# Kernel optimization log

Hardware: AMD Instinct MI355X
Metric: run time of the kernel (lower is better)

The kernel has to match this reference:

```python
import jax, jax.numpy as jnp
import numpy as np

# B batch, N seq (n_vec), V vocab, D model dim, H heads, DH head dim,
# L depth, WS window size, R landmark rank, C classes
B, N, V, D, H, DH, L, WS, R, C = 4, 4096, 512, 512, 8, 64, 4, 128, 256, 10
FF = 4 * D
SCALE = DH ** -0.5


def _ln(t, g, b, eps=1e-5):
    mu = jnp.mean(t, axis=-1, keepdims=True)
    var = jnp.var(t, axis=-1, keepdims=True)
    return (t - mu) * jax.lax.rsqrt(var + eps) * g + b


def setup_inputs():
    key = jax.random.key(0)
    ks = iter(jax.random.split(key, 16))

    def w(shape, s=0.02):
        return (jax.random.normal(next(ks), shape) * s).astype(jnp.float32)

    return dict(
        x=jax.random.randint(next(ks), (B, N), 0, V, dtype=jnp.int32),
        tok_emb=w((V, D)), pos_emb=w((N, D)),
        ln1_g=jnp.ones((L, D), jnp.float32), ln1_b=jnp.zeros((L, D), jnp.float32),
        Wq=w((L, D, H * DH)), Wkv=w((L, D, 2 * H * DH)), Wp=w((L, DH, R)),
        lln_g=jnp.ones((L, DH), jnp.float32), lln_b=jnp.zeros((L, DH), jnp.float32),
        gln_g=jnp.ones((L, DH), jnp.float32), gln_b=jnp.zeros((L, DH), jnp.float32),
        Wo=w((L, H * DH, D)), bo=jnp.zeros((L, D), jnp.float32),
        ln2_g=jnp.ones((L, D), jnp.float32), ln2_b=jnp.zeros((L, D), jnp.float32),
        W1=w((L, D, FF)), b1=jnp.zeros((L, FF), jnp.float32),
        W2=w((L, FF, D)), b2=jnp.zeros((L, D), jnp.float32),
        lnf_g=jnp.ones((D,), jnp.float32), lnf_b=jnp.zeros((D,), jnp.float32),
        Wlog=w((D, V)), blog=jnp.zeros((V,), jnp.float32),
        Wfin=w((N * V, C), 0.005), bfin=jnp.zeros((C,), jnp.float32),
    )


def _forward(x, tok_emb, pos_emb, ln1_g, ln1_b, Wq, Wkv, Wp, lln_g, lln_b,
             gln_g, gln_b, Wo, bo, ln2_g, ln2_b, W1, b1, W2, b2,
             lnf_g, lnf_b, Wlog, blog, Wfin, bfin):
    h = tok_emb[x] + pos_emb[None, :, :]  # [B,N,D]
    nw = N // WS
    for l in range(L):
        # ---- PreNorm Long-Short attention ----
        y = _ln(h, ln1_g[l], ln1_b[l])
        q = (y @ Wq[l]).reshape(B, N, H, DH).transpose(0, 2, 1, 3) * SCALE  # [B,H,N,DH]
        kv = (y @ Wkv[l]).reshape(B, N, 2, H, DH).transpose(2, 0, 3, 1, 4)
        k, v = kv[0], kv[1]  # [B,H,N,DH]
        # dynamic low-rank landmark projection: softmax over the sequence dim
        p = jax.nn.softmax(jnp.einsum('bhnd,dr->bhnr', k, Wp[l]), axis=2)
        gk = _ln(jnp.einsum('bhnr,bhnd->bhrd', p, k), gln_g[l], gln_b[l])  # [B,H,R,DH]
        gv = _ln(jnp.einsum('bhnr,bhnd->bhrd', p, v), gln_g[l], gln_b[l])
        # DualLN on the short-range (local window) keys/values
        lk = _ln(k, lln_g[l], lln_b[l]).reshape(B, H, nw, WS, DH)
        lv = _ln(v, lln_g[l], lln_b[l]).reshape(B, H, nw, WS, DH)
        lq = q.reshape(B, H, nw, WS, DH)
        sim_l = jnp.einsum('bhnwd,bhnxd->bhnwx', lq, lk)  # [B,H,nw,WS,WS]
        sim_g = jnp.einsum('bhnwd,bhrd->bhnwr', lq, gk)   # [B,H,nw,WS,R]
        attn = jax.nn.softmax(jnp.concatenate([sim_l, sim_g], axis=-1), axis=-1)
        a_l, a_g = attn[..., :WS], attn[..., WS:]
        o = (jnp.einsum('bhnwx,bhnxd->bhnwd', a_l, lv)
             + jnp.einsum('bhnwr,bhrd->bhnwd', a_g, gv))
        o = o.reshape(B, H, N, DH).transpose(0, 2, 1, 3).reshape(B, N, H * DH)
        h = h + o @ Wo[l] + bo[l]
        # ---- PreNorm FeedForward ----
        y = _ln(h, ln2_g[l], ln2_b[l])
        h = h + jax.nn.gelu(y @ W1[l] + b1[l]) @ W2[l] + b2[l]
    logits = _ln(h, lnf_g, lnf_b) @ Wlog + blog  # [B,N,V]
    # FLATTEN pooling head (dropout is identity in eval mode)
    return logits.reshape(B, N * V) @ Wfin + bfin  # [B,C]


def reference(x, tok_emb, pos_emb, ln1_g, ln1_b, Wq, Wkv, Wp, lln_g, lln_b,
              gln_g, gln_b, Wo, bo, ln2_g, ln2_b, W1, b1, W2, b2,
              lnf_g, lnf_b, Wlog, blog, Wfin, bfin):
    return _forward(x, tok_emb, pos_emb, ln1_g, ln1_b, Wq, Wkv, Wp, lln_g, lln_b,
                    gln_g, gln_b, Wo, bo, ln2_g, ln2_b, W1, b1, W2, b2,
                    lnf_g, lnf_b, Wlog, blog, Wfin, bfin)
```

## Files before the change

kernel.cpp:

```cpp
#include <hip/hip_runtime.h>
#include <hip/hip_bf16.h>

typedef unsigned short u16;
typedef __attribute__((ext_vector_type(8))) short short8;
typedef __attribute__((ext_vector_type(4))) float floatx4;

#define FLAG_GELU   1
#define FLAG_ACC    2
#define FLAG_NN     4
#define FLAG_CF32   8
#define FLAG_ATOMIC 16

__device__ __forceinline__ float bf2f(u16 u){
  union { unsigned u; float f; } c; c.u = ((unsigned)u)<<16; return c.f;
}
__device__ __forceinline__ u16 f2bf(float f){
  union { float f; unsigned u; } c; c.f = f;
  unsigned r = (c.u + 0x7fffu + ((c.u>>16)&1u))>>16;
  return (u16)r;
}
__device__ __forceinline__ float rdin(const void* base, long long idx, int flagv){
  return flagv ? ((const float*)base)[idx] : bf2f(((const u16*)base)[idx]);
}
__device__ __forceinline__ float fast_gelu(float x){
  float u = 0.7978845608028654f*(x + 0.044715f*x*x*x);
  float e = __expf(2.f*u);
  float t = 1.f - 2.f/(e+1.f);
  return 0.5f*x*(1.f+t);
}

__global__ void detect_kernel(const void* tok, int* flag){
  __shared__ int cnt;
  if(threadIdx.x==0) cnt=0;
  __syncthreads();
  float v = fabsf(bf2f(((const u16*)tok)[threadIdx.x]));
  int bad = (v < 1e3f) ? 0 : 1;
  atomicAdd(&cnt, bad);
  __syncthreads();
  if(threadIdx.x==0) *flag = (cnt>0) ? 1 : 0;
}

__global__ void cvtT_kernel(const void* src, long long off0, long long zstride, u16* __restrict__ dst,
    long long dzstride, int K, int N, const int* flag){
  __shared__ float tl[32][33];
  int fl = *flag;
  int k0 = blockIdx.x*32, n0 = blockIdx.y*32;
  long long base = off0 + (long long)blockIdx.z*zstride;
  for(int i=threadIdx.y;i<32;i+=8){
    long long idx = base + (long long)(k0+i)*N + n0 + threadIdx.x;
    tl[i][threadIdx.x] = fl ? ((const float*)src)[idx] : bf2f(((const u16*)src)[idx]);
  }
  __syncthreads();
  u16* dz = dst + (long long)blockIdx.z*dzstride;
  for(int i=threadIdx.y;i<32;i+=8)
    dz[(long long)(n0+i)*K + k0 + threadIdx.x] = f2bf(tl[threadIdx.x][i]);
}

__global__ void transposeB_kernel(const u16* __restrict__ in, u16* __restrict__ out,
    long long izs0, long long izs1, int zd, long long ozstride, int ldin, int ldout){
  __shared__ u16 tl[32][33];
  int z = blockIdx.z; int z0 = z/zd, z1 = z - z0*zd;
  const u16* ip = in + z0*izs0 + z1*izs1;
  u16* op = out + (long long)z*ozstride;
  int r0 = blockIdx.x*32, c0 = blockIdx.y*32;
  for(int i=threadIdx.y;i<32;i+=8)
    tl[i][threadIdx.x] = ip[(long long)(r0+i)*ldin + c0 + threadIdx.x];
  __syncthreads();
  for(int i=threadIdx.y;i<32;i+=8)
    op[(long long)(c0+i)*ldout + r0 + threadIdx.x] = tl[threadIdx.x][i];
}

__global__ __launch_bounds__(256) void zerof_kernel(float* p, int n){
  int i = blockIdx.x*256 + threadIdx.x;
  if(i<n) p[i]=0.f;
}

struct GemmP {
  const u16* A; const u16* B; float* Cf; u16* Ch;
  const void* bias; int biasOff; const int* dflag;
  int K, lda, ldb, ldc;
  long long sA0,sA1,sA2,sB0,sB1,sB2,sC0,sC1,sC2;
  int d0,d1; float alpha; int flags; int ksplit;
};

__global__ __launch_bounds__(256) void gemm_kernel(GemmP p){
  __shared__ __align__(16) u16 As[64][40];
  __shared__ __align__(16) u16 Bs[64][40];
  int z = blockIdx.z;
  int i0 = z / p.d0; int rem = z - i0*p.d0; int i1 = rem / p.d1; int i2 = rem - i1*p.d1;
  const u16* A  = p.A + i0*p.sA0 + i1*p.sA1 + i2*p.sA2;
  const u16* Bp = p.B + i0*p.sB0 + i1*p.sB1 + i2*p.sB2;
  long long cb = i0*p.sC0 + i1*p.sC1 + i2*p.sC2;
  int kbeg = 0, kend = p.K;
  if(p.ksplit){ kbeg = i2*p.ksplit; kend = kbeg + p.ksplit; }
  int m0 = blockIdx.x*64, n0 = blockIdx.y*64;
  int t = threadIdx.x, lane = t&63, wave = t>>6;
  int wm = (wave>>1)*32, wn = (wave&1)*32;
  int quad = lane>>4, l16 = lane&15;
  floatx4 zero4 = {0.f,0.f,0.f,0.f};
  floatx4 acc00=zero4, acc01=zero4, acc10=zero4, acc11=zero4;
  int sr = t>>2, sc = (t&3)*8;
  int bkr = t>>3, bnc = (t&7)*8;
  bool nn = (p.flags & FLAG_NN);
  for(int k0=kbeg;k0<kend;k0+=32){
    uint4 av = *(const uint4*)(A + (long long)(m0+sr)*p.lda + (k0+sc));
    uint4 bv;
    if(nn) bv = *(const uint4*)(Bp + (long long)(k0+bkr)*p.ldb + (n0+bnc));
    else   bv = *(const uint4*)(Bp + (long long)(n0+sr)*p.ldb + (k0+sc));
    *(uint4*)&As[sr][sc] = av;
    if(nn){
      u16 tmp[8]; *(uint4*)tmp = bv;
      #pragma unroll
      for(int j=0;j<8;j++) Bs[bnc+j][bkr] = tmp[j];
    } else {
      *(uint4*)&Bs[sr][sc] = bv;
    }
    __syncthreads();
    short8 a0 = *(const short8*)&As[wm+l16][quad*8];
    short8 a1 = *(const short8*)&As[wm+16+l16][quad*8];
    short8 b0 = *(const short8*)&Bs[wn+l16][quad*8];
    short8 b1 = *(const short8*)&Bs[wn+16+l16][quad*8];
    acc00 = __builtin_amdgcn_mfma_f32_16x16x32_bf16(a0,b0,acc00,0,0,0);
    acc01 = __builtin_amdgcn_mfma_f32_16x16x32_bf16(a0,b1,acc01,0,0,0);
    acc10 = __builtin_amdgcn_mfma_f32_16x16x32_bf16(a1,b0,acc10,0,0,0);
    acc11 = __builtin_amdgcn_mfma_f32_16x16x32_bf16(a1,b1,acc11,0,0,0);
    __syncthreads();
  }
  int flagv = p.bias ? *p.dflag : 0;
  #pragma unroll
  for(int mi=0;mi<2;mi++){
    #pragma unroll
    for(int ni=0;ni<2;ni++){
      floatx4 a = (mi==0)?((ni==0)?acc00:acc01):((ni==0)?acc10:acc11);
      int cg = n0 + wn + ni*16 + l16;
      float bv_ = p.bias ? rdin(p.bias, (long long)p.biasOff + cg, flagv) : 0.f;
      #pragma unroll
      for(int e=0;e<4;e++){
        int rg = m0 + wm + mi*16 + quad*4 + e;
        float v = a[e]*p.alpha + bv_;
        if(p.flags & FLAG_GELU) v = fast_gelu(v);
        long long ci = cb + (long long)rg*p.ldc + cg;
        if(p.flags & FLAG_ATOMIC){
          atomicAdd(&p.Cf[ci], v);
        } else if(p.flags & FLAG_CF32){
          float o2 = v; if(p.flags&FLAG_ACC) o2 += p.Cf[ci];
          p.Cf[ci] = o2;
        } else {
          float o2 = v; if(p.flags&FLAG_ACC) o2 += bf2f(p.Ch[ci]);
          p.Ch[ci] = f2bf(o2);
        }
      }
    }
  }
}

struct Gemm128P {
  const u16* A; const u16* B; float* Cf; u16* Ch;
  const void* bias; int biasOff; const int* dflag;
  int K, lda, ldb, ldc; float alpha; int flags;
};

template<int BM>
__global__ __launch_bounds__(512) void gemm2ph_kernel(Gemm128P p){
  constexpr int NA   = BM/64;
  constexpr int HH   = BM/2;
  constexpr int MI   = HH/16;
  constexpr int ABUF = BM*64;
  constexpr int LDSZ = (BM==256) ? 69632 : 49152;
  __shared__ __align__(16) u16 lds[LDSZ];
  u16* As = lds;
  u16* Bs = lds + 2*ABUF;
  int m0 = blockIdx.x*BM, n0 = blockIdx.y*256;
  int t = threadIdx.x, lane = t&63, wave = t>>6;
  int quad = lane>>4, l16 = lane&15;
  int wr = wave>>2, wc = wave&3;
  int rowA = t>>3;
  int colk = (((t&7) ^ (rowA&7)))*8;
  const u16* Asrc[NA];
  const u16* Bsrc[4];
  #pragma unroll
  for(int q=0;q<NA;q++) Asrc[q] = p.A + (long long)(m0 + q*64 + rowA)*p.lda + colk;
  #pragma unroll
  for(int q=0;q<4;q++)  Bsrc[q] = p.B + (long long)(n0 + q*64 + rowA)*p.ldb + colk;
  int nk = p.K >> 6;
  floatx4 acc[MI][4] = {};

  auto stage = [&](int buf, int k0){
    #pragma unroll
    for(int q=0;q<NA;q++)
      __builtin_amdgcn_global_load_lds(
        (const __attribute__((address_space(1))) unsigned int*)(Asrc[q] + k0),
        (__attribute__((address_space(3))) unsigned int*)(As + buf*ABUF + q*4096 + wave*512),
        16, 0, 0);
    #pragma unroll
    for(int q=0;q<4;q++)
      __builtin_amdgcn_global_load_lds(
        (const __attribute__((address_space(1))) unsigned int*)(Bsrc[q] + k0),
        (__attribute__((address_space(3))) unsigned int*)(Bs + buf*16384 + q*4096 + wave*512),
        16, 0, 0);
  };

  stage(0, 0);
  __syncthreads();
  int sw = l16&7;
  for(int kt=0; kt<nk; ++kt){
    int cur = kt&1;
    if(kt+1 < nk) stage(cur^1, (kt+1)*64);
    const u16* Ab = As + cur*ABUF;
    const u16* Bb = Bs + cur*16384;
    #pragma unroll
    for(int ks=0; ks<2; ks++){
      short8 a[MI], b[4];
      #pragma unroll
      for(int i=0;i<MI;i++)
        a[i] = *(const short8*)&Ab[(wr*HH + i*16 + l16)*64 + ((((ks<<2)|quad) ^ sw)<<3)];
      #pragma unroll
      for(int j=0;j<4;j++)
        b[j] = *(const short8*)&Bb[(wc*64 + j*16 + l16)*64 + ((((ks<<2)|quad) ^ sw)<<3)];
      #pragma unroll
      for(int i=0;i<MI;i++)
        #pragma unroll
        for(int j=0;j<4;j++)
          acc[i][j] = __builtin_amdgcn_mfma_f32_16x16x32_bf16(a[i], b[j], acc[i][j],0,0,0);
    }
    __syncthreads();
  }

  int flagv = p.bias ? *p.dflag : 0;
  if(!(p.flags & FLAG_CF32)){
    u16* Ct = lds + wave*(HH*68);
    #pragma unroll
    for(int j=0;j<4;j++){
      int cg = n0 + wc*64 + j*16 + l16;
      float bv_ = p.bias ? rdin(p.bias, (long long)p.biasOff + cg, flagv) : 0.f;
      #pragma unroll
      for(int i=0;i<MI;i++){
        #pragma unroll
        for(int e=0;e<4;e++){
          float v = acc[i][j][e]*p.alpha + bv_;
          if(p.flags & FLAG_GELU) v = fast_gelu(v);
          Ct[(i*16 + quad*4 + e)*68 + j*16 + l16] = f2bf(v);
        }
      }
    }
    int rsub = lane>>3, csub = (lane&7)*8;
    #pragma unroll
    for(int rr=0; rr<HH/8; rr++){
      int row = rr*8 + rsub;
      uint4 v = *(const uint4*)&Ct[row*68 + csub];
      *(uint4*)(p.Ch + (long long)(m0 + wr*HH + row)*p.ldc + (n0 + wc*64 + csub)) = v;
    }
  } else {
    #pragma unroll
    for(int j=0;j<4;j++){
      int cg = n0 + wc*64 + j*16 + l16;
      float bv_ = p.bias ? rdin(p.bias, (long long)p.biasOff + cg, flagv) : 0.f;
      #pragma unroll
      for(int i=0;i<MI;i++){
        #pragma unroll
        for(int e=0;e<4;e++){
          int rg = m0 + wr*HH + i*16 + quad*4 + e;
          float v = acc[i][j][e]*p.alpha + bv_;
          if(p.flags & FLAG_GELU) v = fast_gelu(v);
          long long ci = (long long)rg*p.ldc + cg;
          float o2 = v; if(p.flags&FLAG_ACC) o2 += p.Cf[ci];
          p.Cf[ci] = o2;
        }
      }
    }
  }
}

struct AttnP {
  const u16* q;
  const u16* k;
  const u16* gk;
  const u16* vT;
  const u16* gvT;
  u16* o;
};

__global__ __launch_bounds__(256) void attn_kernel(AttnP p){
  __shared__ __align__(16) u16 S[32*392];
  __shared__ float ssum[32];
  const int SST = 392;
  int qb = blockIdx.x;
  int bh = blockIdx.y;
  int b = bh>>3, hh = bh&7;
  int w = qb>>2;
  int t = threadIdx.x, lane = t&63, wave = t>>6;
  int quad = lane>>4, l16 = lane&15;
  int mbase = qb*32;
  short8 aq[2][2];
  #pragma unroll
  for(int mt=0;mt<2;mt++)
    #pragma unroll
    for(int kc=0;kc<2;kc++)
      aq[mt][kc] = *(const short8*)(p.q + ((long long)b*4096 + mbase + mt*16 + l16)*512 + hh*64 + kc*32 + quad*8);
  #pragma unroll
  for(int i=0;i<6;i++){
    int ct = wave*6 + i;
    short8 bf0, bf1;
    if(ct<8){
      const u16* kr = p.k + ((long long)b*4096 + w*128 + ct*16 + l16)*1024 + hh*64;
      bf0 = *(const short8*)(kr + quad*8);
      bf1 = *(const short8*)(kr + 32 + quad*8);
    } else {
      const u16* gr = p.gk + ((long long)bh*256 + (ct-8)*16 + l16)*64;
      bf0 = *(const short8*)(gr + quad*8);
      bf1 = *(const short8*)(gr + 32 + quad*8);
    }
    #pragma unroll
    for(int mt=0;mt<2;mt++){
      floatx4 acc = {0.f,0.f,0.f,0.f};
      acc = __builtin_amdgcn_mfma_f32_16x16x32_bf16(aq[mt][0], bf0, acc,0,0,0);
      acc = __builtin_amdgcn_mfma_f32_16x16x32_bf16(aq[mt][1], bf1, acc,0,0,0);
      #pragma unroll
      for(int e=0;e<4;e++)
        S[(mt*16 + quad*4 + e)*SST + ct*16 + l16] = f2bf(acc[e]);
    }
  }
  __syncthreads();
  {
    int r = t>>3, seg = t&7;
    u16* Srow = S + r*SST + seg*48;
    u16 buf[48];
    #pragma unroll
    for(int it=0; it<6; it++)
      *(uint4*)(buf + it*8) = *(const uint4*)(Srow + it*8);
    float mmax = -3.4e38f;
    #pragma unroll
    for(int j=0;j<48;j++) mmax = fmaxf(mmax, bf2f(buf[j]));
    mmax = fmaxf(mmax, __shfl_xor(mmax, 1));
    mmax = fmaxf(mmax, __shfl_xor(mmax, 2));
    mmax = fmaxf(mmax, __shfl_xor(mmax, 4));
    float s = 0.f;
    #pragma unroll
    for(int j=0;j<48;j++){ float e_ = __expf(bf2f(buf[j]) - mmax); s += e_; buf[j] = f2bf(e_); }
    #pragma unroll
    for(int it=0; it<6; it++)
      *(uint4*)(Srow + it*8) = *(const uint4*)(buf + it*8);
    s += __shfl_xor(s, 1);
    s += __shfl_xor(s, 2);
    s += __shfl_xor(s, 4);
    if(seg==0) ssum[r] = 1.f/s;
  }
  __syncthreads();
  int dt = wave;
  floatx4 oacc[2] = {};
  for(int kc=0; kc<12; kc++){
    short8 ap0 = *(const short8*)(S + (l16)*SST + kc*32 + quad*8);
    short8 ap1 = *(const short8*)(S + (16 + l16)*SST + kc*32 + quad*8);
    short8 bv;
    if(kc<4)
      bv = *(const short8*)(p.vT + (long long)bh*262144 + (dt*16+l16)*4096 + w*128 + kc*32 + quad*8);
    else
      bv = *(const short8*)(p.gvT + (long long)bh*16384 + (dt*16+l16)*256 + (kc-4)*32 + quad*8);
    oacc[0] = __builtin_amdgcn_mfma_f32_16x16x32_bf16(ap0, bv, oacc[0],0,0,0);
    oacc[1] = __builtin_amdgcn_mfma_f32_16x16x32_bf16(ap1, bv, oacc[1],0,0,0);
  }
  #pragma unroll
  for(int mt=0;mt<2;mt++){
    #pragma unroll
    for(int e=0;e<4;e++){
      int row = mt*16 + quad*4 + e;
      float inv = ssum[row];
      p.o[((long long)b*4096 + mbase + row)*512 + hh*64 + dt*16 + l16] = f2bf(oacc[mt][e]*inv);
    }
  }
}

__global__ __launch_bounds__(256) void embed_kernel(const int* __restrict__ x, const void* tok,
    const void* pos, float* __restrict__ h, const int* flag){
  int i = blockIdx.x*256 + threadIdx.x;
  int flagv = *flag;
  int d = i & 511;
  int n = (i>>9) & 4095;
  int bn = i>>9;
  int tid2 = x[bn];
  h[i] = rdin(tok, (long long)tid2*512 + d, flagv) + rdin(pos, (long long)n*512 + d, flagv);
}

__global__ __launch_bounds__(256) void ln512_kernel(const float* __restrict__ h,
    const void* g, const void* b, int goff, u16* __restrict__ y, const int* flag){
  int row = blockIdx.x;
  int flagv = *flag;
  const float* hr = h + (size_t)row*512;
  int t = threadIdx.x;
  float x0 = hr[t], x1 = hr[t+256];
  float s1 = x0+x1, s2 = x0*x0+x1*x1;
  for(int o=32;o>0;o>>=1){ s1 += __shfl_down(s1,o,64); s2 += __shfl_down(s2,o,64); }
  __shared__ float sh1[4], sh2[4];
  int wv=t>>6, ln=t&63;
  if(ln==0){ sh1[wv]=s1; sh2[wv]=s2; }
  __syncthreads();
  float st = sh1[0]+sh1[1]+sh1[2]+sh1[3];
  float qt = sh2[0]+sh2[1]+sh2[2]+sh2[3];
  float mu = st*(1.f/512.f);
  float var = qt*(1.f/512.f) - mu*mu;
  float inv = rsqrtf(var+1e-5f);
  u16* yr = y + (size_t)row*512;
  yr[t]     = f2bf((x0-mu)*inv*rdin(g,goff+t,flagv)     + rdin(b,goff+t,flagv));
  yr[t+256] = f2bf((x1-mu)*inv*rdin(g,goff+t+256,flagv) + rdin(b,goff+t+256,flagv));
}

__global__ __launch_bounds__(256) void ln64_kernel(const u16* __restrict__ in, const float* __restrict__ inF,
    u16* __restrict__ out, const void* g, const void* b, int goff,
    long long s0, long long s1v, long long s2v, int d0, int d1, const int* flag){
  int r = blockIdx.x*4 + (threadIdx.x>>6);
  int ln = threadIdx.x&63;
  int flagv = *flag;
  int i0 = r/d0; int rem = r - i0*d0; int i1 = rem/d1; int i2 = rem - i1*d1;
  long long off = i0*s0 + i1*s1v + i2*s2v;
  float x = inF ? inF[off+ln] : bf2f(in[off + ln]);
  float s = x, sq = x*x;
  for(int o=32;o>0;o>>=1){ s += __shfl_down(s,o,64); sq += __shfl_down(sq,o,64); }
  s = __shfl(s,0,64); sq = __shfl(sq,0,64);
  float mu = s*(1.f/64.f), var = sq*(1.f/64.f)-mu*mu;
  float inv = rsqrtf(var+1e-5f);
  out[off + ln] = f2bf((x-mu)*inv*rdin(g,goff+ln,flagv) + rdin(b,goff+ln,flagv));
}

__global__ __launch_bounds__(256) void softmax4096_kernel(u16* __restrict__ p){
  u16* pr = p + (size_t)blockIdx.x*4096;
  int t = threadIdx.x;
  u16 tmp[16];
  *(uint4*)tmp     = *(const uint4*)(pr + t*16);
  *(uint4*)(tmp+8) = *(const uint4*)(pr + t*16 + 8);
  float xs[16]; float m=-3.4e38f;
  #pragma unroll
  for(int i=0;i<16;i++){ xs[i]=bf2f(tmp[i]); m=fmaxf(m,xs[i]); }
  for(int o=32;o>0;o>>=1) m = fmaxf(m, __shfl_down(m,o,64));
  __shared__ float sm[4]; __shared__ float sv[4];
  int wv=t>>6, ln=t&63;
  if(ln==0) sm[wv]=m;
  __syncthreads();
  m = fmaxf(fmaxf(sm[0],sm[1]),fmaxf(sm[2],sm[3]));
  float s=0;
  #pragma unroll
  for(int i=0;i<16;i++){ xs[i]=__expf(xs[i]-m); s+=xs[i]; }
  for(int o=32;o>0;o>>=1) s += __shfl_down(s,o,64);
  if(ln==0) sv[wv]=s;
  __syncthreads();
  s = sv[0]+sv[1]+sv[2]+sv[3];
  float inv = 1.f/s;
  #pragma unroll
  for(int i=0;i<16;i++) tmp[i]=f2bf(xs[i]*inv);
  *(uint4*)(pr + t*16)     = *(uint4*)tmp;
  *(uint4*)(pr + t*16 + 8) = *(uint4*)(tmp+8);
}

__global__ void zero40_kernel(float* p){ if(threadIdx.x<40) p[threadIdx.x]=0.f; }

__global__ __launch_bounds__(256) void head_kernel(const float* __restrict__ logits,
    const void* wfin, float* __restrict__ part, const int* flag){
  int b = blockIdx.x>>8, chunk = blockIdx.x&255;
  int flagv = *flag;
  const float* lr = logits + (size_t)b*2097152 + (size_t)chunk*8192;
  long long jbase = (long long)chunk*8192;
  float acc[10];
  #pragma unroll
  for(int c=0;c<10;c++) acc[c]=0.f;
  for(int it=0; it<16; ++it){
    int jp = it*256 + threadIdx.x;
    float2 lv = *(const float2*)(lr + jp*2);
    long long wrow = (jbase + (long long)jp*2)*10;
    if(flagv){
      const float* w = (const float*)wfin + wrow;
      #pragma unroll
      for(int c=0;c<10;c++) acc[c] += lv.x*w[c] + lv.y*w[c+10];
    } else {
      const unsigned* wu = (const unsigned*)((const u16*)wfin + wrow);
      unsigned wd[10];
      #pragma unroll
      for(int k2=0;k2<10;k2++) wd[k2] = wu[k2];
      #pragma unroll
      for(int c=0;c<10;c++){
        unsigned lo = wd[c>>1], hi = wd[5+(c>>1)];
        float w0 = bf2f((u16)((c&1)? (lo>>16) : (lo&0xffffu)));
        float w1 = bf2f((u16)((c&1)? (hi>>16) : (hi&0xffffu)));
        acc[c] += lv.x*w0 + lv.y*w1;
      }
    }
  }
  __shared__ float red[4];
  int wv=threadIdx.x>>6, ln=threadIdx.x&63;
  for(int c=0;c<10;c++){
    float v=acc[c];
    for(int o=32;o>0;o>>=1) v+=__shfl_down(v,o,64);
    __syncthreads();
    if(ln==0) red[wv]=v;
    __syncthreads();
    if(threadIdx.x==0) atomicAdd(&part[b*10+c], red[0]+red[1]+red[2]+red[3]);
  }
}

__global__ void fin_kernel(const float* __restrict__ part, const void* bfin, void* out, const int* flag){
  int i=threadIdx.x;
  int flagv = *flag;
  if(i<40){
    float r = part[i] + rdin(bfin, i%10, flagv);
    if(flagv) ((float*)out)[i] = r;
    else      ((u16*)out)[i]   = f2bf(r);
  }
}

static const size_t OFF_H    = 0;
static const size_t OFF_Y    = 33554432;
static const size_t OFF_GKF  = 33554432;
static const size_t OFF_GVF  = 35651584;
static const size_t OFF_Q    = 50331648;
static const size_t OFF_KV   = 67108864;
static const size_t OFF_GK   = 100663296;
static const size_t OFF_GV   = 101711872;
static const size_t OFF_BIG  = 102760448;
static const size_t OFF_KT   = 169869312;
static const size_t OFF_VT   = 186646528;
static const size_t OFF_WTP  = 203423744;
static const size_t OFF_WQT  = 203554816;
static const size_t OFF_WKVT = 204079104;
static const size_t OFF_WOT  = 205127680;
static const size_t OFF_W1T  = 205651968;
static const size_t OFF_W2T  = 207749120;
static const size_t OFF_PART = 209846272;
static const size_t OFF_FLAG = 209846528;
static const size_t WS_NEED  = 209846784;

static inline GemmP mkg(const void*A,const void*B,void*C,const void*bias,int biasOff,const int* dflag,
  int K,int lda,int ldb,int ldc,
  long long a0,long long a1,long long a2,long long b0,long long b1,long long b2,
  long long c0,long long c1,long long c2,int d0,int d1,float alpha,int flags,int ksplit){
  GemmP p; p.A=(const u16*)A; p.B=(const u16*)B;
  p.Cf=(float*)C; p.Ch=(u16*)C; p.bias=bias; p.biasOff=biasOff; p.dflag=dflag;
  p.K=K;p.lda=lda;p.ldb=ldb;p.ldc=ldc;
  p.sA0=a0;p.sA1=a1;p.sA2=a2;p.sB0=b0;p.sB1=b1;p.sB2=b2;p.sC0=c0;p.sC1=c1;p.sC2=c2;
  p.d0=d0;p.d1=d1;p.alpha=alpha;p.flags=flags;p.ksplit=ksplit; return p;
}
static inline Gemm128P mk128(const void*A,const void*B,void*C,const void*bias,int biasOff,const int* dflag,
  int K,int lda,int ldb,int ldc,float alpha,int flags){
  Gemm128P p; p.A=(const u16*)A; p.B=(const u16*)B;
  p.Cf=(float*)C; p.Ch=(u16*)C; p.bias=bias; p.biasOff=biasOff; p.dflag=dflag;
  p.K=K;p.lda=lda;p.ldb=ldb;p.ldc=ldc;p.alpha=alpha;p.flags=flags; return p;
}

extern "C" void kernel_launch(void* const* d_in, const int* in_sizes, int n_in,
                              void* d_out, int out_size, void* d_ws, size_t ws_size,
                              hipStream_t stream){
  (void)in_sizes;(void)n_in;(void)out_size;
  if(ws_size < WS_NEED) return;
  const int*  x    = (const int*)d_in[0];
  const void* tok  = d_in[1];
  const void* pos  = d_in[2];
  const void* ln1g = d_in[3];
  const void* ln1b = d_in[4];
  const void* Wq   = d_in[5];
  const void* Wkv  = d_in[6];
  const void* Wp   = d_in[7];
  const void* llng = d_in[8];
  const void* llnb = d_in[9];
  const void* glng = d_in[10];
  const void* glnb = d_in[11];
  const void* Wo   = d_in[12];
  const void* bo   = d_in[13];
  const void* ln2g = d_in[14];
  const void* ln2b = d_in[15];
  const void* W1   = d_in[16];
  const void* b1   = d_in[17];
  const void* W2   = d_in[18];
  const void* b2   = d_in[19];
  const void* lnfg = d_in[20];
  const void* lnfb = d_in[21];
  const void* Wlog = d_in[22];
  const void* blog = d_in[23];
  const void* Wfin = d_in[24];
  const void* bfin = d_in[25];

  char* ws = (char*)d_ws;
  float* h    = (float*)(ws + OFF_H);
  u16* y      = (u16*)(ws + OFF_Y);
  u16* ob     = (u16*)(ws + OFF_Y);
  float* gkF  = (float*)(ws + OFF_GKF);
  float* gvF  = (float*)(ws + OFF_GVF);
  u16* qb     = (u16*)(ws + OFF_Q);
  u16* kv     = (u16*)(ws + OFF_KV);
  u16* gk     = (u16*)(ws + OFF_GK);
  u16* gv     = (u16*)(ws + OFF_GV);
  u16* big    = (u16*)(ws + OFF_BIG);
  float* bigf = (float*)(ws + OFF_BIG);
  u16* gvT    = (u16*)(ws + OFF_KT);
  u16* vT     = (u16*)(ws + OFF_VT);
  u16* wTp    = (u16*)(ws + OFF_WTP);
  u16* sWqT   = (u16*)(ws + OFF_WQT);
  u16* sWkvT  = (u16*)(ws + OFF_WKVT);
  u16* sWoT   = (u16*)(ws + OFF_WOT);
  u16* sW1T   = (u16*)(ws + OFF_W1T);
  u16* sW2T   = (u16*)(ws + OFF_W2T);
  float* part = (float*)(ws + OFF_PART);
  int* flag   = (int*)(ws + OFF_FLAG);

  dim3 tb(32,8);
  detect_kernel<<<dim3(1),dim3(256),0,stream>>>(tok, flag);
  cvtT_kernel<<<dim3(2,8,4),tb,0,stream>>>(Wp, 0, 16384, wTp, 16384, 64, 256, flag);
  embed_kernel<<<dim3(32768),dim3(256),0,stream>>>(x, tok, pos, h, flag);

  for(int l=0;l<4;l++){
    cvtT_kernel<<<dim3(16,16,1),tb,0,stream>>>(Wq,  (long long)l*262144,  0, sWqT,  0, 512, 512,  flag);
    cvtT_kernel<<<dim3(16,32,1),tb,0,stream>>>(Wkv, (long long)l*524288,  0, sWkvT, 0, 512, 1024, flag);
    cvtT_kernel<<<dim3(16,16,1),tb,0,stream>>>(Wo,  (long long)l*262144,  0, sWoT,  0, 512, 512,  flag);
    cvtT_kernel<<<dim3(16,64,1),tb,0,stream>>>(W1,  (long long)l*1048576, 0, sW1T,  0, 512, 2048, flag);
    cvtT_kernel<<<dim3(64,16,1),tb,0,stream>>>(W2,  (long long)l*1048576, 0, sW2T,  0, 2048, 512, flag);

    ln512_kernel<<<dim3(16384),dim3(256),0,stream>>>(h, ln1g, ln1b, l*512, y, flag);
    { Gemm128P p = mk128(y, sWqT, qb, nullptr,0,flag, 512,512,512,512, 0.125f, 0);
      gemm2ph_kernel<128><<<dim3(128,2),512,0,stream>>>(p); }
    { Gemm128P p = mk128(y, sWkvT, kv, nullptr,0,flag, 512,512,512,1024, 1.f, 0);
      gemm2ph_kernel<256><<<dim3(64,4),512,0,stream>>>(p); }
    zerof_kernel<<<dim3(4096),dim3(256),0,stream>>>(gkF, 1048576);
    { GemmP p = mkg(wTp + (size_t)l*16384, kv, big, nullptr,0,flag, 64,64,1024,4096,
        0,0,0, 4194304LL,64,0, 8388608LL,1048576LL,0, 8,1, 1.f, 0, 0);
      gemm_kernel<<<dim3(4,64,32),256,0,stream>>>(p); }
    softmax4096_kernel<<<dim3(8192),dim3(256),0,stream>>>(big);
    { GemmP p = mkg(big, kv, gkF, nullptr,0,flag, 4096,4096,1024,64,
        8388608LL,1048576LL,0, 4194304LL,64,0, 131072LL,16384LL,0, 64,8, 1.f,
        FLAG_CF32|FLAG_ATOMIC|FLAG_NN, 512);
      gemm_kernel<<<dim3(4,1,256),256,0,stream>>>(p); }
    { GemmP p = mkg(big, kv+512, gvF, nullptr,0,flag, 4096,4096,1024,64,
        8388608LL,1048576LL,0, 4194304LL,64,0, 131072LL,16384LL,0, 64,8, 1.f,
        FLAG_CF32|FLAG_ATOMIC|FLAG_NN, 512);
      gemm_kernel<<<dim3(4,1,256),256,0,stream>>>(p); }
    ln64_kernel<<<dim3(2048),dim3(256),0,stream>>>(gk, gkF, gk, glng, glnb, l*64, 64,1,1, 1,1, flag);
    ln64_kernel<<<dim3(2048),dim3(256),0,stream>>>(gv, gvF, gv, glng, glnb, l*64, 64,1,1, 1,1, flag);
    ln64_kernel<<<dim3(32768),dim3(256),0,stream>>>(kv,     nullptr, kv,     llng, llnb, l*64, 4194304LL,64,1024, 32768,4096, flag);
    ln64_kernel<<<dim3(32768),dim3(256),0,stream>>>(kv+512, nullptr, kv+512, llng, llnb, l*64, 4194304LL,64,1024, 32768,4096, flag);
    transposeB_kernel<<<dim3(128,2,32),tb,0,stream>>>(kv+512, vT, 4194304LL,64,8, 262144LL, 1024, 4096);
    transposeB_kernel<<<dim3(8,2,32),tb,0,stream>>>(gv, gvT, 16384LL,0,1, 16384LL, 64, 256);
    { AttnP ap; ap.q=qb; ap.k=kv; ap.gk=gk; ap.vT=vT; ap.gvT=gvT; ap.o=ob;
      attn_kernel<<<dim3(128,32),256,0,stream>>>(ap); }
    { Gemm128P p = mk128(ob, sWoT, h, bo,l*512,flag, 512,512,512,512, 1.f, FLAG_ACC|FLAG_CF32);
      gemm2ph_kernel<128><<<dim3(128,2),512,0,stream>>>(p); }
    ln512_kernel<<<dim3(16384),dim3(256),0,stream>>>(h, ln2g, ln2b, l*512, y, flag);
    { Gemm128P p = mk128(y, sW1T, big, b1,l*2048,flag, 512,512,512,2048, 1.f, FLAG_GELU);
      gemm2ph_kernel<256><<<dim3(64,8),512,0,stream>>>(p); }
    { Gemm128P p = mk128(big, sW2T, h, b2,l*512,flag, 2048,2048,2048,512, 1.f, FLAG_ACC|FLAG_CF32);
      gemm2ph_kernel<128><<<dim3(128,2),512,0,stream>>>(p); }
  }
  ln512_kernel<<<dim3(16384),dim3(256),0,stream>>>(h, lnfg, lnfb, 0, y, flag);
  cvtT_kernel<<<dim3(16,16,1),tb,0,stream>>>(Wlog, 0, 0, sWqT, 0, 512, 512, flag);
  { Gemm128P p = mk128(y, sWqT, bigf, blog,0,flag, 512,512,512,512, 1.f, FLAG_CF32);
    gemm2ph_kernel<128><<<dim3(128,2),512,0,stream>>>(p); }
  zero40_kernel<<<dim3(1),dim3(64),0,stream>>>(part);
  head_kernel<<<dim3(1024),dim3(256),0,stream>>>(bigf, Wfin, part, flag);
  fin_kernel<<<dim3(1),dim3(64),0,stream>>>(part, bfin, d_out, flag);
}
```

Baseline: 2.347 ms.

## Reuse Wfin tile across all batches in head kernel via shared memory

```diff
diff --git a/kernel.cpp b/kernel.cpp
--- a/kernel.cpp
+++ b/kernel.cpp
@@ -454,45 +454,69 @@
 
 __global__ __launch_bounds__(256) void head_kernel(const float* __restrict__ logits,
     const void* wfin, float* __restrict__ part, const int* flag){
-  int b = blockIdx.x>>8, chunk = blockIdx.x&255;
+  __shared__ __align__(16) u16 Wl[20480];
+  __shared__ float redl[4][40];
   int flagv = *flag;
-  const float* lr = logits + (size_t)b*2097152 + (size_t)chunk*8192;
-  long long jbase = (long long)chunk*8192;
-  float acc[10];
-  #pragma unroll
-  for(int c=0;c<10;c++) acc[c]=0.f;
-  for(int it=0; it<16; ++it){
-    int jp = it*256 + threadIdx.x;
-    float2 lv = *(const float2*)(lr + jp*2);
-    long long wrow = (jbase + (long long)jp*2)*10;
-    if(flagv){
-      const float* w = (const float*)wfin + wrow;
-      #pragma unroll
-      for(int c=0;c<10;c++) acc[c] += lv.x*w[c] + lv.y*w[c+10];
-    } else {
-      const unsigned* wu = (const unsigned*)((const u16*)wfin + wrow);
-      unsigned wd[10];
-      #pragma unroll
-      for(int k2=0;k2<10;k2++) wd[k2] = wu[k2];
+  int t = threadIdx.x;
+  long long rbase = (long long)blockIdx.x*2048;
+  float acc[4][10];
+  #pragma unroll
+  for(int b4=0;b4<4;b4++)
+    #pragma unroll
+    for(int c=0;c<10;c++) acc[b4][c]=0.f;
+
+  if(!flagv){
+    const uint4* src = (const uint4*)((const u16*)wfin + rbase*10);
+    uint4* dst = (uint4*)Wl;
+    #pragma unroll
+    for(int i=0;i<10;i++) dst[t + i*256] = src[t + i*256];
+    __syncthreads();
+    const unsigned* Wd = (const unsigned*)Wl;
+    #pragma unroll
+    for(int i=0;i<8;i++){
+      int r = t + i*256;
+      float l0 = logits[rbase + r];
+      float l1 = logits[2097152 + rbase + r];
+      float l2 = logits[4194304 + rbase + r];
+      float l3 = logits[6291456 + rbase + r];
+      #pragma unroll
+      for(int k2=0;k2<5;k2++){
+        unsigned d = Wd[r*5 + k2];
+        float w0 = bf2f((u16)(d & 0xffffu));
+        float w1 = bf2f((u16)(d >> 16));
+        acc[0][2*k2]   += l0*w0; acc[0][2*k2+1] += l0*w1;
+        acc[1][2*k2]   += l1*w0; acc[1][2*k2+1] += l1*w1;
+        acc[2][2*k2]   += l2*w0; acc[2][2*k2+1] += l2*w1;
+        acc[3][2*k2]   += l3*w0; acc[3][2*k2+1] += l3*w1;
+      }
+    }
+  } else {
+    #pragma unroll
+    for(int i=0;i<8;i++){
+      int r = t + i*256;
+      float l0 = logits[rbase + r];
+      float l1 = logits[2097152 + rbase + r];
+      float l2 = logits[4194304 + rbase + r];
+      float l3 = logits[6291456 + rbase + r];
+      const float* wr = (const float*)wfin + (rbase + r)*10;
       #pragma unroll
       for(int c=0;c<10;c++){
-        unsigned lo = wd[c>>1], hi = wd[5+(c>>1)];
-        float w0 = bf2f((u16)((c&1)? (lo>>16) : (lo&0xffffu)));
-        float w1 = bf2f((u16)((c&1)? (hi>>16) : (hi&0xffffu)));
-        acc[c] += lv.x*w0 + lv.y*w1;
+        float w = wr[c];
+        acc[0][c] += l0*w; acc[1][c] += l1*w; acc[2][c] += l2*w; acc[3][c] += l3*w;
       }
     }
   }
-  __shared__ float red[4];
-  int wv=threadIdx.x>>6, ln=threadIdx.x&63;
-  for(int c=0;c<10;c++){
-    float v=acc[c];
-    for(int o=32;o>0;o>>=1) v+=__shfl_down(v,o,64);
-    __syncthreads();
-    if(ln==0) red[wv]=v;
-    __syncthreads();
-    if(threadIdx.x==0) atomicAdd(&part[b*10+c], red[0]+red[1]+red[2]+red[3]);
-  }
+  int wv = t>>6, ln = t&63;
+  #pragma unroll
+  for(int b4=0;b4<4;b4++)
+    #pragma unroll
+    for(int c=0;c<10;c++){
+      float v = acc[b4][c];
+      for(int o=32;o>0;o>>=1) v += __shfl_down(v,o,64);
+      if(ln==0) redl[wv][b4*10+c] = v;
+    }
+  __syncthreads();
+  if(t<40) atomicAdd(&part[t], redl[0][t]+redl[1][t]+redl[2][t]+redl[3][t]);
 }
 
 __global__ void fin_kernel(const float* __restrict__ part, const void* bfin, void* out, const int* flag){
```

Measured after the change: 2.234 ms. 4.8% less time.
